# Performance work log

Measured on AMD Instinct MI355X. Metric: run time of the kernel, lower is better.

## Reference

```python
import jax, jax.numpy as jnp
import numpy as np
import math

H = 128
W = 128
N = 2048
DIM = 768
TWO_PI = 2.0 * math.pi
ALPHA_MIN = 1.0 / 255.0


def setup_inputs() -> dict:
    key = jax.random.key(0)
    ks = jax.random.split(key, 6)
    # _xyz = atanh(2*(rand-0.5)); clip uniform away from endpoints to avoid inf
    u = jax.random.uniform(ks[0], (N, 2), minval=1e-4, maxval=1.0 - 1e-4)
    xyz = jnp.arctanh(2.0 * (u - 0.5))
    scaling = jax.random.uniform(ks[1], (N, 2))
    rotation = jax.random.uniform(ks[2], (N, 1))
    features = jax.random.uniform(ks[3], (N, 3))
    opacity = jnp.ones((N, 1), jnp.float32)
    w_up = jax.random.normal(ks[4], (DIM, 3), jnp.float32) * 0.05
    b_up = jnp.zeros((DIM,), jnp.float32)
    x = jax.random.normal(ks[5], (1, DIM, H, W), jnp.float32)
    return {"x": x, "xyz": xyz, "scaling": scaling, "rotation": rotation,
            "features": features, "opacity": opacity, "w_up": w_up, "b_up": b_up}


def _forward(xyz, scaling, rotation, features, opacity, w_up, b_up):
    # activations (get_xyz / get_scaling / get_rotation)
    means = jnp.tanh(xyz)                                   # [N,2] in (-1,1)
    s = jnp.abs(scaling + 0.5)                              # [N,2]
    theta = jax.nn.sigmoid(rotation[:, 0]) * TWO_PI         # [N]
    c, sn = jnp.cos(theta), jnp.sin(theta)
    # M = R(theta) @ diag(s); cov2d = M M^T
    a = c * s[:, 0]; b = -sn * s[:, 1]
    d = sn * s[:, 0]; e = c * s[:, 1]
    cov_xx = a * a + b * b
    cov_xy = a * d + b * e
    cov_yy = d * d + e * e
    det = cov_xx * cov_yy - cov_xy * cov_xy
    # conic = inverse covariance (A, B, C)
    A = cov_yy / det; B = -cov_xy / det; C = cov_xx / det   # [N]
    # project [-1,1] -> pixel centers
    gx = 0.5 * (means[:, 0] + 1.0) * W                      # [N]
    gy = 0.5 * (means[:, 1] + 1.0) * H
    px = jnp.arange(W, dtype=jnp.float32) + 0.5
    py = jnp.arange(H, dtype=jnp.float32) + 0.5
    PX, PY = jnp.meshgrid(px, py)                           # [H,W], PX varies along W
    dx = gx[None, :] - PX.reshape(-1)[:, None]              # [P,N], P=H*W
    dy = gy[None, :] - PY.reshape(-1)[:, None]
    sigma = 0.5 * (A * dx * dx + C * dy * dy) + B * dx * dy # [P,N]
    alpha = jnp.minimum(0.999, opacity[:, 0][None, :] * jnp.exp(-sigma))
    alpha = jnp.where((sigma < 0.0) | (alpha < ALPHA_MIN), 0.0, alpha)
    # summation rasterizer: per-pixel weighted sum of colors
    img = jnp.clip(alpha @ features, 0.0, 1.0)              # [P,3]
    feat = img @ w_up.T + b_up                              # [P,DIM]
    return feat.T.reshape(1, DIM, H, W)


def reference(x, xyz, scaling, rotation, features, opacity, w_up, b_up):
    del x  # only its channel dim (== DIM) shapes the output in the original
    return _forward(xyz, scaling, rotation, features, opacity, w_up, b_up)
```

## Files before the change

### kernel.cpp

```cpp
#include <hip/hip_runtime.h>
#include <math.h>

#define HH 128
#define WW 128
#define NG 2048
#define DIMV 768
#define PIX (HH * WW)
#define A_MIN (1.0f / 255.0f)
#define TW 16
#define TH 4
#define NT 512
#define NWV 8
#define CH 256
#define TWO_PI 6.28318530717958647692f

__global__ __launch_bounds__(NT) void fused_kernel(
    const float* __restrict__ xyz, const float* __restrict__ scaling,
    const float* __restrict__ rotation, const float* __restrict__ features,
    const float* __restrict__ opacity, const float* __restrict__ w_up,
    const float* __restrict__ b_up, float* __restrict__ out)
{
    __shared__ int s_cnt;
    __shared__ int s_idx[NG];
    __shared__ float4 cA[CH];
    __shared__ float4 cB[CH];
    __shared__ float2 cC[CH];
    __shared__ float s_red[NWV * 64 * 3];
    __shared__ __align__(16) float s_r[64];
    __shared__ __align__(16) float s_g[64];
    __shared__ __align__(16) float s_b[64];

    int tid = threadIdx.x;
    int bx = blockIdx.x & 7, by = blockIdx.x >> 3;
    int px0 = bx * TW, py0 = by * TH;

    if (tid == 0) s_cnt = 0;
    __syncthreads();

    {
        float x0 = px0 + 0.5f, x1 = px0 + TW - 0.5f;
        float y0 = py0 + 0.5f, y1 = py0 + TH - 0.5f;
        #pragma unroll
        for (int g0 = 0; g0 < NG; g0 += NT) {
            int g = g0 + tid;
            float2 xz = ((const float2*)xyz)[g];
            float e2x = __expf(2.0f * xz.x);
            float e2y = 2.0f * __expf(2.0f * xz.y);
            float gx = (e2x / (e2x + 1.0f)) * (float)WW;
            float gy = (e2y / (e2y + 2.0f)) * (float)HH;
            float2 sc = ((const float2*)scaling)[g];
            float s0 = fabsf(sc.x + 0.5f);
            float s1 = fabsf(sc.y + 0.5f);
            float trc = s0 * s0 + s1 * s1;
            float L = __logf(255.0f * opacity[g]);
            float r2 = (L > 0.0f) ? 2.0f * L * trc * 1.0002f + 1e-3f : -1.0f;
            float ddx = fmaxf(fmaxf(x0 - gx, gx - x1), 0.0f);
            float ddy = fmaxf(fmaxf(y0 - gy, gy - y1), 0.0f);
            if (ddx * ddx + ddy * ddy <= r2) {
                int pos = atomicAdd(&s_cnt, 1);
                s_idx[pos] = g;
            }
        }
    }
    __syncthreads();
    int cnt = s_cnt;

    int lane = tid & 63, wv = tid >> 6;
    float pxf = px0 + (lane & 15) + 0.5f;
    float pyf = py0 + (lane >> 4) + 0.5f;
    float ar = 0.0f, ag = 0.0f, ab = 0.0f;

    for (int ck = 0; ck < cnt; ck += CH) {
        int csz = min(CH, cnt - ck);
        for (int j = tid; j < csz; j += NT) {
            int g = s_idx[ck + j];
            float2 xz = ((const float2*)xyz)[g];
            float e2x = __expf(2.0f * xz.x);
            float e2y = 2.0f * __expf(2.0f * xz.y);
            float gx = (e2x / (e2x + 1.0f)) * (float)WW;
            float gy = (e2y / (e2y + 2.0f)) * (float)HH;
            float2 sc = ((const float2*)scaling)[g];
            float s0 = fabsf(sc.x + 0.5f);
            float s1 = fabsf(sc.y + 0.5f);
            float th = TWO_PI / (1.0f + __expf(-rotation[g]));
            float sn = __sinf(th), cs = __cosf(th);
            float a = cs * s0, b = -sn * s1, d = sn * s0, e = cs * s1;
            float cxx = a * a + b * b;
            float cxy = a * d + b * e;
            float cyy = d * d + e * e;
            float inv = 1.0f / (cxx * cyy - cxy * cxy);
            float op = opacity[g];
            cA[j] = make_float4(0.5f * cyy * inv, -cxy * inv, 0.5f * cxx * inv, op);
            cB[j] = make_float4(gx, gy, features[3 * g + 0], features[3 * g + 1]);
            cC[j] = make_float2(features[3 * g + 2], 0.0f);
        }
        __syncthreads();
        for (int k = wv; k < csz; k += NWV) {
            float4 a0 = cA[k];
            float4 a1 = cB[k];
            float2 a2 = cC[k];
            float dx = a1.x - pxf, dy = a1.y - pyf;
            float sig = fmaf(a0.y * dx, dy, fmaf(a0.x * dx, dx, a0.z * dy * dy));
            float al = fminf(0.999f, a0.w * __expf(-sig));
            al = (sig < 0.0f || al < A_MIN) ? 0.0f : al;
            ar = fmaf(al, a1.z, ar);
            ag = fmaf(al, a1.w, ag);
            ab = fmaf(al, a2.x, ab);
        }
        __syncthreads();
    }

    s_red[(wv * 64 + lane) * 3 + 0] = ar;
    s_red[(wv * 64 + lane) * 3 + 1] = ag;
    s_red[(wv * 64 + lane) * 3 + 2] = ab;
    __syncthreads();
    if (tid < 64) {
        float sr = 0.0f, sg = 0.0f, sb = 0.0f;
        #pragma unroll
        for (int w = 0; w < NWV; ++w) {
            sr += s_red[(w * 64 + tid) * 3 + 0];
            sg += s_red[(w * 64 + tid) * 3 + 1];
            sb += s_red[(w * 64 + tid) * 3 + 2];
        }
        s_r[tid] = fminf(1.0f, fmaxf(0.0f, sr));
        s_g[tid] = fminf(1.0f, fmaxf(0.0f, sg));
        s_b[tid] = fminf(1.0f, fmaxf(0.0f, sb));
    }
    __syncthreads();

    int q = tid & 15, dbase = tid >> 4;
    int row = q >> 2, c4 = q & 3;
    float4 r4 = *(const float4*)&s_r[row * 16 + c4 * 4];
    float4 g4 = *(const float4*)&s_g[row * 16 + c4 * 4];
    float4 b4 = *(const float4*)&s_b[row * 16 + c4 * 4];
    size_t pofs = (size_t)(py0 + row) * WW + px0 + c4 * 4;
    for (int i = 0; i < DIMV / 32; ++i) {
        int d = dbase + (i << 5);
        float w0 = w_up[3 * d + 0], w1 = w_up[3 * d + 1], w2 = w_up[3 * d + 2];
        float bb = b_up[d];
        float4 v;
        v.x = fmaf(w0, r4.x, fmaf(w1, g4.x, fmaf(w2, b4.x, bb)));
        v.y = fmaf(w0, r4.y, fmaf(w1, g4.y, fmaf(w2, b4.y, bb)));
        v.z = fmaf(w0, r4.z, fmaf(w1, g4.z, fmaf(w2, b4.z, bb)));
        v.w = fmaf(w0, r4.w, fmaf(w1, g4.w, fmaf(w2, b4.w, bb)));
        *(float4*)(out + (size_t)d * PIX + pofs) = v;
    }
}

extern "C" void kernel_launch(void* const* d_in, const int* in_sizes, int n_in,
                              void* d_out, int out_size, void* d_ws, size_t ws_size,
                              hipStream_t stream)
{
    const float* xyz      = (const float*)d_in[1];
    const float* scaling  = (const float*)d_in[2];
    const float* rotation = (const float*)d_in[3];
    const float* features = (const float*)d_in[4];
    const float* opacity  = (const float*)d_in[5];
    const float* w_up     = (const float*)d_in[6];
    const float* b_up     = (const float*)d_in[7];
    (void)d_ws; (void)ws_size;

    fused_kernel<<<256, NT, 0, stream>>>(xyz, scaling, rotation, features,
                                         opacity, w_up, b_up, (float*)d_out);
}
```

Measured before the change: 126.6 us.

## Split fused kernel into raster and channel-projection kernels via workspace image

Splits the fused kernel in two. The first kernel rasterizes only and writes the clamped RGB image to workspace. A separate, widely parallel kernel (3072 blocks) then projects each pixel to the 768 output channels with contiguous float4 stores. The aim is to spread the large output write (about 50 MB) across many more blocks than the 256 raster blocks, in exchange for a second launch and a small round trip of the image through global memory.

```diff
diff --git a/kernel.cpp b/kernel.cpp
--- a/kernel.cpp
+++ b/kernel.cpp
@@ -14,11 +14,10 @@
 #define CH 256
 #define TWO_PI 6.28318530717958647692f
 
-__global__ __launch_bounds__(NT) void fused_kernel(
+__global__ __launch_bounds__(NT) void raster_kernel(
     const float* __restrict__ xyz, const float* __restrict__ scaling,
     const float* __restrict__ rotation, const float* __restrict__ features,
-    const float* __restrict__ opacity, const float* __restrict__ w_up,
-    const float* __restrict__ b_up, float* __restrict__ out)
+    const float* __restrict__ opacity, float* __restrict__ img)
 {
     __shared__ int s_cnt;
     __shared__ int s_idx[NG];
@@ -26,9 +25,6 @@
     __shared__ float4 cB[CH];
     __shared__ float2 cC[CH];
     __shared__ float s_red[NWV * 64 * 3];
-    __shared__ __align__(16) float s_r[64];
-    __shared__ __align__(16) float s_g[64];
-    __shared__ __align__(16) float s_b[64];
 
     int tid = threadIdx.x;
     int bx = blockIdx.x & 7, by = blockIdx.x >> 3;
@@ -122,28 +118,35 @@
             sg += s_red[(w * 64 + tid) * 3 + 1];
             sb += s_red[(w * 64 + tid) * 3 + 2];
         }
-        s_r[tid] = fminf(1.0f, fmaxf(0.0f, sr));
-        s_g[tid] = fminf(1.0f, fmaxf(0.0f, sg));
-        s_b[tid] = fminf(1.0f, fmaxf(0.0f, sb));
+        int p = (py0 + (tid >> 4)) * WW + px0 + (tid & 15);
+        img[p]           = fminf(1.0f, fmaxf(0.0f, sr));
+        img[PIX + p]     = fminf(1.0f, fmaxf(0.0f, sg));
+        img[2 * PIX + p] = fminf(1.0f, fmaxf(0.0f, sb));
     }
-    __syncthreads();
+}
 
-    int q = tid & 15, dbase = tid >> 4;
-    int row = q >> 2, c4 = q & 3;
-    float4 r4 = *(const float4*)&s_r[row * 16 + c4 * 4];
-    float4 g4 = *(const float4*)&s_g[row * 16 + c4 * 4];
-    float4 b4 = *(const float4*)&s_b[row * 16 + c4 * 4];
-    size_t pofs = (size_t)(py0 + row) * WW + px0 + c4 * 4;
-    for (int i = 0; i < DIMV / 32; ++i) {
-        int d = dbase + (i << 5);
+__global__ __launch_bounds__(256) void project_kernel(
+    const float* __restrict__ img, const float* __restrict__ w_up,
+    const float* __restrict__ b_up, float* __restrict__ out)
+{
+    int grp = blockIdx.x >> 4;
+    int seg = blockIdx.x & 15;
+    int p = seg * 1024 + threadIdx.x * 4;
+    float4 r = *(const float4*)(img + p);
+    float4 g = *(const float4*)(img + PIX + p);
+    float4 b = *(const float4*)(img + 2 * PIX + p);
+    int d0 = grp * 4;
+    #pragma unroll
+    for (int i = 0; i < 4; ++i) {
+        int d = d0 + i;
         float w0 = w_up[3 * d + 0], w1 = w_up[3 * d + 1], w2 = w_up[3 * d + 2];
         float bb = b_up[d];
         float4 v;
-        v.x = fmaf(w0, r4.x, fmaf(w1, g4.x, fmaf(w2, b4.x, bb)));
-        v.y = fmaf(w0, r4.y, fmaf(w1, g4.y, fmaf(w2, b4.y, bb)));
-        v.z = fmaf(w0, r4.z, fmaf(w1, g4.z, fmaf(w2, b4.z, bb)));
-        v.w = fmaf(w0, r4.w, fmaf(w1, g4.w, fmaf(w2, b4.w, bb)));
-        *(float4*)(out + (size_t)d * PIX + pofs) = v;
+        v.x = fmaf(w0, r.x, fmaf(w1, g.x, fmaf(w2, b.x, bb)));
+        v.y = fmaf(w0, r.y, fmaf(w1, g.y, fmaf(w2, b.y, bb)));
+        v.z = fmaf(w0, r.z, fmaf(w1, g.z, fmaf(w2, b.z, bb)));
+        v.w = fmaf(w0, r.w, fmaf(w1, g.w, fmaf(w2, b.w, bb)));
+        *(float4*)(out + (size_t)d * PIX + p) = v;
     }
 }
 
@@ -158,8 +161,10 @@
     const float* opacity  = (const float*)d_in[5];
     const float* w_up     = (const float*)d_in[6];
     const float* b_up     = (const float*)d_in[7];
-    (void)d_ws; (void)ws_size;
+    float* out = (float*)d_out;
+    float* img = (float*)d_ws;
 
-    fused_kernel<<<256, NT, 0, stream>>>(xyz, scaling, rotation, features,
-                                         opacity, w_up, b_up, (float*)d_out);
+    raster_kernel<<<256, NT, 0, stream>>>(xyz, scaling, rotation, features,
+                                          opacity, img);
+    project_kernel<<<(DIMV / 4) * 16, 256, 0, stream>>>(img, w_up, b_up, out);
 }
```

After: 109.2 us. 13.7% less time.
